# Kernel tuning notes

Measured on AMD Instinct MI355X. Metric: run time of the kernel, lower is better.

Reference implementation:

```python
import jax, jax.numpy as jnp
import numpy as np

N = 50000      # nodes per graph
E = 800000     # edges per graph
IN_DIM = 64
HIDDEN = 128
OUT_DIM = 2
P = 100000     # candidate residue pairs


def setup_inputs() -> dict:
    key = jax.random.key(0)
    ks = jax.random.split(key, 12)
    x1 = jax.random.normal(ks[0], (N, IN_DIM), dtype=jnp.float32)
    x2 = jax.random.normal(ks[1], (N, IN_DIM), dtype=jnp.float32)
    edge_index1 = jax.random.randint(ks[2], (2, E), 0, N, dtype=jnp.int64)
    edge_index2 = jax.random.randint(ks[3], (2, E), 0, N, dtype=jnp.int64)
    label = jax.random.randint(ks[4], (P, 2), 0, N, dtype=jnp.int64)
    s = 0.05
    W0 = jax.random.normal(ks[5], (IN_DIM, HIDDEN), dtype=jnp.float32) * s
    W1 = jax.random.normal(ks[6], (HIDDEN, HIDDEN), dtype=jnp.float32) * s
    W2 = jax.random.normal(ks[7], (HIDDEN, HIDDEN), dtype=jnp.float32) * s
    b0 = jnp.zeros((HIDDEN,), dtype=jnp.float32)
    b1 = jnp.zeros((HIDDEN,), dtype=jnp.float32)
    b2 = jnp.zeros((HIDDEN,), dtype=jnp.float32)
    fcW = jax.random.normal(ks[8], (2 * HIDDEN, OUT_DIM), dtype=jnp.float32) * s
    fcb = jnp.zeros((OUT_DIM,), dtype=jnp.float32)
    return {"x1": x1, "edge_index1": edge_index1, "x2": x2,
            "edge_index2": edge_index2, "label": label,
            "W0": W0, "b0": b0, "W1": W1, "b1": b1, "W2": W2, "b2": b2,
            "fcW": fcW, "fcb": fcb}


def gcn_conv(x, src, dst, W, b):
    """PyG GCNConv: linear, add self-loops, symmetric D^-1/2 (A+I) D^-1/2 aggregation."""
    n = x.shape[0]
    h = x @ W                                   # [n, out]
    loops = jnp.arange(n, dtype=src.dtype)
    src_sl = jnp.concatenate([src, loops])      # [E+n]
    dst_sl = jnp.concatenate([dst, loops])
    deg = jax.ops.segment_sum(jnp.ones_like(src_sl, dtype=h.dtype), dst_sl,
                              num_segments=n)
    dinv = jax.lax.rsqrt(jnp.maximum(deg, 1.0e-12))
    norm = dinv[src_sl] * dinv[dst_sl]          # [E+n]
    msgs = h[src_sl] * norm[:, None]            # gather + scale
    out = jax.ops.segment_sum(msgs, dst_sl, num_segments=n)  # scatter-add
    return out + b


def gcn_tower(x, edge_index, params):
    src, dst = edge_index[0], edge_index[1]
    for (W, b) in params:
        x = jax.nn.relu(gcn_conv(x, src, dst, W, b))
    return x


def reference(x1, edge_index1, x2, edge_index2, label,
              W0, b0, W1, b1, W2, b2, fcW, fcb):
    params = [(W0, b0), (W1, b1), (W2, b2)]
    x_ligand = gcn_tower(x1, edge_index1, params)    # shared GCN weights
    x_receptor = gcn_tower(x2, edge_index2, params)
    x = jnp.concatenate([x_ligand[label[:, 0]], x_receptor[label[:, 1]]], axis=1)
    return jax.nn.relu(x @ fcW + fcb)
```

## Files before the change

### kernel.cpp

```cpp
#include <hip/hip_runtime.h>
#include <math.h>



__global__ void histU_kernel(const int* __restrict__ d1, const int* __restrict__ d2,
                             int* __restrict__ cnt, int E, int N) {
    int i = blockIdx.x * blockDim.x + threadIdx.x;
    if (i < E) atomicAdd(&cnt[d1[i]], 1);
    else if (i < 2 * E) atomicAdd(&cnt[N + d2[i - E]], 1);
}

__global__ __launch_bounds__(256) void block_reduce_kernel(const int* __restrict__ cnt,
                                                           float* __restrict__ dinv,
                                                           int* __restrict__ blockSums, int NN) {
    int i = blockIdx.x * 256 + threadIdx.x;
    int v = 0;
    if (i < NN) {
        v = cnt[i];
        dinv[i] = 1.0f / sqrtf((float)(v + 1));
    }
    int s = v;
#pragma unroll
    for (int o = 32; o; o >>= 1) s += __shfl_down(s, o);
    __shared__ int ws[4];
    if ((threadIdx.x & 63) == 0) ws[threadIdx.x >> 6] = s;
    __syncthreads();
    if (threadIdx.x == 0) blockSums[blockIdx.x] = ws[0] + ws[1] + ws[2] + ws[3];
}

__global__ __launch_bounds__(1024) void scan_sums_kernel(const int* __restrict__ blockSums,
                                                         int* __restrict__ blockOff, int nb,
                                                         int* __restrict__ rowptr, int NN) {
    __shared__ int sh[1024];
    int t = threadIdx.x;
    int v = (t < nb) ? blockSums[t] : 0;
    sh[t] = v;
    __syncthreads();
    for (int o = 1; o < 1024; o <<= 1) {
        int u = (t >= o) ? sh[t - o] : 0;
        __syncthreads();
        sh[t] += u;
        __syncthreads();
    }
    if (t < nb) blockOff[t] = sh[t] - v;
    if (t == 1023) rowptr[NN] = sh[1023];
}

__global__ __launch_bounds__(256) void scan_write_kernel(const int* __restrict__ cnt,
                                                         const int* __restrict__ blockOff,
                                                         int* __restrict__ rowptr, int NN) {
    __shared__ int sh[256];
    int i = blockIdx.x * 256 + threadIdx.x;
    int t = threadIdx.x;
    int v = (i < NN) ? cnt[i] : 0;
    sh[t] = v;
    __syncthreads();
    for (int o = 1; o < 256; o <<= 1) {
        int u = (t >= o) ? sh[t - o] : 0;
        __syncthreads();
        sh[t] += u;
        __syncthreads();
    }
    if (i < NN) rowptr[i] = blockOff[blockIdx.x] + sh[t] - v;
}

__global__ void placeU_kernel(const int* __restrict__ s1, const int* __restrict__ d1,
                              const int* __restrict__ s2, const int* __restrict__ d2,
                              const int* __restrict__ rowptr, int* __restrict__ cnt,
                              int* __restrict__ csr, int E, int N) {
    int i = blockIdx.x * blockDim.x + threadIdx.x;
    int s, d;
    if (i < E)          { s = s1[i];         d = d1[i]; }
    else if (i < 2 * E) { s = s2[i - E] + N; d = d2[i - E] + N; }
    else return;
    int p = atomicSub(&cnt[d], 1);
    csr[rowptr[d] + p - 1] = s;
}


__global__ void agg64U_kernel(const float* __restrict__ x1, const float* __restrict__ x2,
                              const int* __restrict__ rowptr, const int* __restrict__ csr,
                              const float* __restrict__ dinv, float* __restrict__ S,
                              int NN, int N) {
    int w = blockIdx.x * (blockDim.x >> 6) + (threadIdx.x >> 6);
    int lane = threadIdx.x & 63;
    if (w >= NN) return;
    int beg = rowptr[w], end = rowptr[w + 1];
    const float* selfrow = (w < N) ? (x1 + (size_t)w * 64) : (x2 + (size_t)(w - N) * 64);
    float acc = dinv[w] * selfrow[lane];
    int e = beg;
    for (; e + 8 <= end; e += 8) {
        int s0 = csr[e], s1 = csr[e + 1], s2 = csr[e + 2], s3 = csr[e + 3];
        int s4 = csr[e + 4], s5 = csr[e + 5], s6 = csr[e + 6], s7 = csr[e + 7];
        const float* r0 = (s0 < N) ? (x1 + (size_t)s0 * 64) : (x2 + (size_t)(s0 - N) * 64);
        const float* r1 = (s1 < N) ? (x1 + (size_t)s1 * 64) : (x2 + (size_t)(s1 - N) * 64);
        const float* r2 = (s2 < N) ? (x1 + (size_t)s2 * 64) : (x2 + (size_t)(s2 - N) * 64);
        const float* r3 = (s3 < N) ? (x1 + (size_t)s3 * 64) : (x2 + (size_t)(s3 - N) * 64);
        const float* r4 = (s4 < N) ? (x1 + (size_t)s4 * 64) : (x2 + (size_t)(s4 - N) * 64);
        const float* r5 = (s5 < N) ? (x1 + (size_t)s5 * 64) : (x2 + (size_t)(s5 - N) * 64);
        const float* r6 = (s6 < N) ? (x1 + (size_t)s6 * 64) : (x2 + (size_t)(s6 - N) * 64);
        const float* r7 = (s7 < N) ? (x1 + (size_t)s7 * 64) : (x2 + (size_t)(s7 - N) * 64);
        float v0 = dinv[s0] * r0[lane];
        float v1 = dinv[s1] * r1[lane];
        float v2 = dinv[s2] * r2[lane];
        float v3 = dinv[s3] * r3[lane];
        float v4 = dinv[s4] * r4[lane];
        float v5 = dinv[s5] * r5[lane];
        float v6 = dinv[s6] * r6[lane];
        float v7 = dinv[s7] * r7[lane];
        acc += ((v0 + v1) + (v2 + v3)) + ((v4 + v5) + (v6 + v7));
    }
    for (; e < end; ++e) {
        int s = csr[e];
        const float* r = (s < N) ? (x1 + (size_t)s * 64) : (x2 + (size_t)(s - N) * 64);
        acc += dinv[s] * r[lane];
    }
    S[(size_t)w * 64 + lane] = acc;
}


__global__ void agg128_kernel(const float* __restrict__ Xf, const int* __restrict__ rowptr,
                              const int* __restrict__ csr, float* __restrict__ Sf, int NN) {
    int w = blockIdx.x * (blockDim.x >> 6) + (threadIdx.x >> 6);
    int lane = threadIdx.x & 63;
    if (w >= NN) return;
    const float2* X = (const float2*)Xf;
    float2* S = (float2*)Sf;
    int beg = rowptr[w], end = rowptr[w + 1];
    float2 self = X[(size_t)w * 64 + lane];
    float ax = self.x, ay = self.y;
    int e = beg;
    for (; e + 8 <= end; e += 8) {
        int s0 = csr[e], s1 = csr[e + 1], s2 = csr[e + 2], s3 = csr[e + 3];
        int s4 = csr[e + 4], s5 = csr[e + 5], s6 = csr[e + 6], s7 = csr[e + 7];
        float2 v0 = X[(size_t)s0 * 64 + lane];
        float2 v1 = X[(size_t)s1 * 64 + lane];
        float2 v2 = X[(size_t)s2 * 64 + lane];
        float2 v3 = X[(size_t)s3 * 64 + lane];
        float2 v4 = X[(size_t)s4 * 64 + lane];
        float2 v5 = X[(size_t)s5 * 64 + lane];
        float2 v6 = X[(size_t)s6 * 64 + lane];
        float2 v7 = X[(size_t)s7 * 64 + lane];
        ax += ((v0.x + v1.x) + (v2.x + v3.x)) + ((v4.x + v5.x) + (v6.x + v7.x));
        ay += ((v0.y + v1.y) + (v2.y + v3.y)) + ((v4.y + v5.y) + (v6.y + v7.y));
    }
    for (; e < end; ++e) {
        float2 v = X[(size_t)csr[e] * 64 + lane];
        ax += v.x; ay += v.y;
    }
    float2 r; r.x = ax; r.y = ay;
    S[(size_t)w * 64 + lane] = r;
}


template <int K>
__global__ __launch_bounds__(256) void gemm_relu(const float* __restrict__ A,
                                                 const float* __restrict__ W,
                                                 const float* __restrict__ B,
                                                 const float* __restrict__ dinv, int post,
                                                 float* __restrict__ C, int M) {
    const int BK = 32;
    __shared__ float As[BK][68];
    __shared__ float Ws[BK][128];

    int t = threadIdx.x;
    int tx = t & 31, ty = t >> 5;
    int row0 = blockIdx.x * 64;

    float acc[8][4];
#pragma unroll
    for (int i = 0; i < 8; ++i)
#pragma unroll
        for (int j = 0; j < 4; ++j) acc[i][j] = 0.f;

    for (int k0 = 0; k0 < K; k0 += BK) {
#pragma unroll
        for (int l = 0; l < 2; ++l) {
            int j = t + l * 256;
            int r = j >> 3, kq = j & 7;
            int gr = row0 + r; if (gr >= M) gr = M - 1;
            float4 v = *reinterpret_cast<const float4*>(A + (size_t)gr * K + k0 + kq * 4);
            As[kq * 4 + 0][r] = v.x;
            As[kq * 4 + 1][r] = v.y;
            As[kq * 4 + 2][r] = v.z;
            As[kq * 4 + 3][r] = v.w;
        }
#pragma unroll
        for (int l = 0; l < 4; ++l) {
            int j = t + l * 256;
            int k = j >> 5, c4 = j & 31;
            *reinterpret_cast<float4*>(&Ws[k][c4 * 4]) =
                *reinterpret_cast<const float4*>(W + (size_t)(k0 + k) * 128 + c4 * 4);
        }
        __syncthreads();
#pragma unroll
        for (int k = 0; k < BK; ++k) {
            float4 w0 = *reinterpret_cast<const float4*>(&Ws[k][tx * 4]);
            float4 a0 = *reinterpret_cast<const float4*>(&As[k][ty * 8]);
            float4 a1 = *reinterpret_cast<const float4*>(&As[k][ty * 8 + 4]);
            float a[8] = {a0.x, a0.y, a0.z, a0.w, a1.x, a1.y, a1.z, a1.w};
            float wv[4] = {w0.x, w0.y, w0.z, w0.w};
#pragma unroll
            for (int i = 0; i < 8; ++i)
#pragma unroll
                for (int j = 0; j < 4; ++j) acc[i][j] += a[i] * wv[j];
        }
        __syncthreads();
    }

    float4 bc = *reinterpret_cast<const float4*>(B + tx * 4);
#pragma unroll
    for (int i = 0; i < 8; ++i) {
        int r = row0 + ty * 8 + i;
        if (r < M) {
            float d = dinv[r];
            float po = post ? d : 1.0f;
            float4 v;
            v.x = fmaxf(acc[i][0] * d + bc.x, 0.f) * po;
            v.y = fmaxf(acc[i][1] * d + bc.y, 0.f) * po;
            v.z = fmaxf(acc[i][2] * d + bc.z, 0.f) * po;
            v.w = fmaxf(acc[i][3] * d + bc.w, 0.f) * po;
            *reinterpret_cast<float4*>(&C[(size_t)r * 128 + tx * 4]) = v;
        }
    }
}


__global__ void fc_kernel(const float* __restrict__ H3, const int* __restrict__ label,
                          const float* __restrict__ fcW, const float* __restrict__ fcb,
                          float* __restrict__ out, int P, int N) {
    int w = blockIdx.x * (blockDim.x >> 6) + (threadIdx.x >> 6);
    int lane = threadIdx.x & 63;
    if (w >= P) return;
    int l0 = label[2 * w], l1 = label[2 * w + 1] + N;
    float xl0 = H3[(size_t)l0 * 128 + lane];
    float xl1 = H3[(size_t)l0 * 128 + 64 + lane];
    float xr0 = H3[(size_t)l1 * 128 + lane];
    float xr1 = H3[(size_t)l1 * 128 + 64 + lane];
    float a0 = xl0 * fcW[lane * 2]             + xl1 * fcW[(64 + lane) * 2]
             + xr0 * fcW[(128 + lane) * 2]     + xr1 * fcW[(192 + lane) * 2];
    float a1 = xl0 * fcW[lane * 2 + 1]         + xl1 * fcW[(64 + lane) * 2 + 1]
             + xr0 * fcW[(128 + lane) * 2 + 1] + xr1 * fcW[(192 + lane) * 2 + 1];
#pragma unroll
    for (int o = 32; o; o >>= 1) {
        a0 += __shfl_xor(a0, o);
        a1 += __shfl_xor(a1, o);
    }
    if (lane == 0) {
        out[2 * w]     = fmaxf(a0 + fcb[0], 0.f);
        out[2 * w + 1] = fmaxf(a1 + fcb[1], 0.f);
    }
}


extern "C" void kernel_launch(void* const* d_in, const int* in_sizes, int n_in,
                              void* d_out, int out_size, void* d_ws, size_t ws_size,
                              hipStream_t stream) {
    const float* x1   = (const float*)d_in[0];
    const int*   e1   = (const int*)d_in[1];
    const float* x2   = (const float*)d_in[2];
    const int*   e2   = (const int*)d_in[3];
    const int*   label= (const int*)d_in[4];
    const float* W0   = (const float*)d_in[5];
    const float* b0   = (const float*)d_in[6];
    const float* W1   = (const float*)d_in[7];
    const float* b1   = (const float*)d_in[8];
    const float* W2   = (const float*)d_in[9];
    const float* b2   = (const float*)d_in[10];
    const float* fcW  = (const float*)d_in[11];
    const float* fcb  = (const float*)d_in[12];
    float* out = (float*)d_out;

    const int N = in_sizes[0] / 64;
    const int E = in_sizes[1] / 2;
    const int P = in_sizes[4] / 2;
    const int NN = 2 * N;
    const int NB = (NN + 255) / 256;

    char* ws = (char*)d_ws;
    size_t off = 0;
    auto alloc = [&](size_t bytes) -> void* {
        void* p = ws + off;
        off += (bytes + 255) & ~(size_t)255;
        return p;
    };
    int*   cnt      = (int*)alloc((size_t)NN * 4);
    int*   rowptr   = (int*)alloc((size_t)(NN + 1) * 4);
    float* dinv     = (float*)alloc((size_t)NN * 4);
    int*   csr      = (int*)alloc((size_t)2 * E * 4);
    int*   blockSums= (int*)alloc((size_t)NB * 4);
    int*   blockOff = (int*)alloc((size_t)NB * 4);
    float* S        = (float*)alloc((size_t)NN * 128 * 4);
    float* Xs       = (float*)alloc((size_t)NN * 128 * 4);

    hipMemsetAsync(cnt, 0, (size_t)NN * 4, stream);
    histU_kernel<<<(2 * E + 255) / 256, 256, 0, stream>>>(e1 + E, e2 + E, cnt, E, N);
    block_reduce_kernel<<<NB, 256, 0, stream>>>(cnt, dinv, blockSums, NN);
    scan_sums_kernel<<<1, 1024, 0, stream>>>(blockSums, blockOff, NB, rowptr, NN);
    scan_write_kernel<<<NB, 256, 0, stream>>>(cnt, blockOff, rowptr, NN);
    placeU_kernel<<<(2 * E + 255) / 256, 256, 0, stream>>>(e1, e1 + E, e2, e2 + E,
                                                           rowptr, cnt, csr, E, N);
    agg64U_kernel<<<(NN + 3) / 4, 256, 0, stream>>>(x1, x2, rowptr, csr, dinv, S, NN, N);
    gemm_relu<64><<<(NN + 63) / 64, 256, 0, stream>>>(S, W0, b0, dinv, 1, Xs, NN);
    agg128_kernel<<<(NN + 3) / 4, 256, 0, stream>>>(Xs, rowptr, csr, S, NN);
    gemm_relu<128><<<(NN + 63) / 64, 256, 0, stream>>>(S, W1, b1, dinv, 1, Xs, NN);
    agg128_kernel<<<(NN + 3) / 4, 256, 0, stream>>>(Xs, rowptr, csr, S, NN);
    gemm_relu<128><<<(NN + 63) / 64, 256, 0, stream>>>(S, W2, b2, dinv, 0, Xs, NN);

    fc_kernel<<<(P + 3) / 4, 256, 0, stream>>>(Xs, label, fcW, fcb, out, P, N);
}
```

Measured before the change: 611.2 us.

## Run GCN dense layers on bf16x3 MFMA with split hi/lo operands

Replaces the FP32 SIMT tiled GEMM with an MFMA 16x16x32 bf16 kernel. It keeps near-fp32 accuracy by splitting activations and weights into bf16 hi/lo pairs and summing three products. The aggregation kernels now write the hi/lo bf16 pair directly, and a small prep kernel splits and transposes the weights. The aggregation tails also become a predicated unrolled loop. This trades extra MFMA work and conversion arithmetic for tensor-core throughput, at some precision risk from the dropped lo*lo term.

```diff
diff --git a/kernel.cpp b/kernel.cpp
--- a/kernel.cpp
+++ b/kernel.cpp
@@ -1,6 +1,17 @@
 #include <hip/hip_runtime.h>
 #include <math.h>
 
+typedef __attribute__((ext_vector_type(8))) short bf16x8;
+typedef __attribute__((ext_vector_type(4))) float f32x4;
+
+__device__ inline unsigned short f2bf(float f) {
+    unsigned int u = __float_as_uint(f);
+    unsigned int r = u + 0x7fffu + ((u >> 16) & 1u);
+    return (unsigned short)(r >> 16);
+}
+__device__ inline float bf2f(unsigned short b) {
+    return __uint_as_float(((unsigned int)b) << 16);
+}
 
 
 __global__ void histU_kernel(const int* __restrict__ d1, const int* __restrict__ d2,
@@ -78,9 +89,30 @@
 }
 
 
+__global__ void prep_weights(const float* __restrict__ W0, const float* __restrict__ W1,
+                             const float* __restrict__ W2,
+                             unsigned short* __restrict__ W0h, unsigned short* __restrict__ W0l,
+                             unsigned short* __restrict__ W1h, unsigned short* __restrict__ W1l,
+                             unsigned short* __restrict__ W2h, unsigned short* __restrict__ W2l) {
+    const float* W; unsigned short *Wh, *Wl; int K;
+    if (blockIdx.x == 0)      { W = W0; Wh = W0h; Wl = W0l; K = 64; }
+    else if (blockIdx.x == 1) { W = W1; Wh = W1h; Wl = W1l; K = 128; }
+    else                      { W = W2; Wh = W2h; Wl = W2l; K = 128; }
+    for (int i = threadIdx.x; i < K * 128; i += 256) {
+        int k = i >> 7, c = i & 127;
+        float v = W[i];
+        unsigned short h = f2bf(v);
+        unsigned short l = f2bf(v - bf2f(h));
+        Wh[c * K + k] = h;
+        Wl[c * K + k] = l;
+    }
+}
+
+
 __global__ void agg64U_kernel(const float* __restrict__ x1, const float* __restrict__ x2,
                               const int* __restrict__ rowptr, const int* __restrict__ csr,
-                              const float* __restrict__ dinv, float* __restrict__ S,
+                              const float* __restrict__ dinv,
+                              unsigned short* __restrict__ Shi, unsigned short* __restrict__ Slo,
                               int NN, int N) {
     int w = blockIdx.x * (blockDim.x >> 6) + (threadIdx.x >> 6);
     int lane = threadIdx.x & 63;
@@ -89,7 +121,8 @@
     const float* selfrow = (w < N) ? (x1 + (size_t)w * 64) : (x2 + (size_t)(w - N) * 64);
     float acc = dinv[w] * selfrow[lane];
     int e = beg;
-    for (; e + 8 <= end; e += 8) {
+    int full_end = beg + ((end - beg) & ~7);
+    for (; e < full_end; e += 8) {
         int s0 = csr[e], s1 = csr[e + 1], s2 = csr[e + 2], s3 = csr[e + 3];
         int s4 = csr[e + 4], s5 = csr[e + 5], s6 = csr[e + 6], s7 = csr[e + 7];
         const float* r0 = (s0 < N) ? (x1 + (size_t)s0 * 64) : (x2 + (size_t)(s0 - N) * 64);
@@ -110,27 +143,37 @@
         float v7 = dinv[s7] * r7[lane];
         acc += ((v0 + v1) + (v2 + v3)) + ((v4 + v5) + (v6 + v7));
     }
-    for (; e < end; ++e) {
-        int s = csr[e];
-        const float* r = (s < N) ? (x1 + (size_t)s * 64) : (x2 + (size_t)(s - N) * 64);
-        acc += dinv[s] * r[lane];
-    }
-    S[(size_t)w * 64 + lane] = acc;
+    if (e < end) {
+#pragma unroll
+        for (int j = 0; j < 7; ++j) {
+            int a = e + j;
+            bool vld = a < end;
+            int s = csr[vld ? a : beg];
+            float wt = vld ? dinv[s] : 0.f;
+            const float* r = (s < N) ? (x1 + (size_t)s * 64) : (x2 + (size_t)(s - N) * 64);
+            acc += wt * r[lane];
+        }
+    }
+    unsigned short h = f2bf(acc);
+    Shi[(size_t)w * 64 + lane] = h;
+    Slo[(size_t)w * 64 + lane] = f2bf(acc - bf2f(h));
 }
 
 
 __global__ void agg128_kernel(const float* __restrict__ Xf, const int* __restrict__ rowptr,
-                              const int* __restrict__ csr, float* __restrict__ Sf, int NN) {
+                              const int* __restrict__ csr,
+                              unsigned short* __restrict__ Shi, unsigned short* __restrict__ Slo,
+                              int NN) {
     int w = blockIdx.x * (blockDim.x >> 6) + (threadIdx.x >> 6);
     int lane = threadIdx.x & 63;
     if (w >= NN) return;
     const float2* X = (const float2*)Xf;
-    float2* S = (float2*)Sf;
     int beg = rowptr[w], end = rowptr[w + 1];
     float2 self = X[(size_t)w * 64 + lane];
     float ax = self.x, ay = self.y;
     int e = beg;
-    for (; e + 8 <= end; e += 8) {
+    int full_end = beg + ((end - beg) & ~7);
+    for (; e < full_end; e += 8) {
         int s0 = csr[e], s1 = csr[e + 1], s2 = csr[e + 2], s3 = csr[e + 3];
         int s4 = csr[e + 4], s5 = csr[e + 5], s6 = csr[e + 6], s7 = csr[e + 7];
         float2 v0 = X[(size_t)s0 * 64 + lane];
@@ -144,83 +187,86 @@
         ax += ((v0.x + v1.x) + (v2.x + v3.x)) + ((v4.x + v5.x) + (v6.x + v7.x));
         ay += ((v0.y + v1.y) + (v2.y + v3.y)) + ((v4.y + v5.y) + (v6.y + v7.y));
     }
-    for (; e < end; ++e) {
-        float2 v = X[(size_t)csr[e] * 64 + lane];
-        ax += v.x; ay += v.y;
-    }
-    float2 r; r.x = ax; r.y = ay;
-    S[(size_t)w * 64 + lane] = r;
+    if (e < end) {
+#pragma unroll
+        for (int j = 0; j < 7; ++j) {
+            int a = e + j;
+            bool vld = a < end;
+            int s = csr[vld ? a : beg];
+            float m = vld ? 1.f : 0.f;
+            float2 v = X[(size_t)s * 64 + lane];
+            ax += m * v.x; ay += m * v.y;
+        }
+    }
+    unsigned short hx = f2bf(ax), hy = f2bf(ay);
+    ushort2 H; H.x = hx; H.y = hy;
+    ushort2 L; L.x = f2bf(ax - bf2f(hx)); L.y = f2bf(ay - bf2f(hy));
+    *reinterpret_cast<ushort2*>(Shi + (size_t)w * 128 + 2 * lane) = H;
+    *reinterpret_cast<ushort2*>(Slo + (size_t)w * 128 + 2 * lane) = L;
 }
 
 
 template <int K>
-__global__ __launch_bounds__(256) void gemm_relu(const float* __restrict__ A,
-                                                 const float* __restrict__ W,
-                                                 const float* __restrict__ B,
+__global__ __launch_bounds__(512) void gemm_mfma(const unsigned short* __restrict__ Ah,
+                                                 const unsigned short* __restrict__ Al,
+                                                 const unsigned short* __restrict__ WhT,
+                                                 const unsigned short* __restrict__ WlT,
+                                                 const float* __restrict__ bias,
                                                  const float* __restrict__ dinv, int post,
                                                  float* __restrict__ C, int M) {
-    const int BK = 32;
-    __shared__ float As[BK][68];
-    __shared__ float Ws[BK][128];
+    const int LDA = K + 8;
+    __shared__ unsigned short lds[2 * 128 * LDA];
+    unsigned short* ldsH = lds;
+    unsigned short* ldsL = lds + 128 * LDA;
 
     int t = threadIdx.x;
-    int tx = t & 31, ty = t >> 5;
-    int row0 = blockIdx.x * 64;
-
-    float acc[8][4];
-#pragma unroll
-    for (int i = 0; i < 8; ++i)
-#pragma unroll
-        for (int j = 0; j < 4; ++j) acc[i][j] = 0.f;
-
-    for (int k0 = 0; k0 < K; k0 += BK) {
-#pragma unroll
-        for (int l = 0; l < 2; ++l) {
-            int j = t + l * 256;
-            int r = j >> 3, kq = j & 7;
-            int gr = row0 + r; if (gr >= M) gr = M - 1;
-            float4 v = *reinterpret_cast<const float4*>(A + (size_t)gr * K + k0 + kq * 4);
-            As[kq * 4 + 0][r] = v.x;
-            As[kq * 4 + 1][r] = v.y;
-            As[kq * 4 + 2][r] = v.z;
-            As[kq * 4 + 3][r] = v.w;
-        }
-#pragma unroll
-        for (int l = 0; l < 4; ++l) {
-            int j = t + l * 256;
-            int k = j >> 5, c4 = j & 31;
-            *reinterpret_cast<float4*>(&Ws[k][c4 * 4]) =
-                *reinterpret_cast<const float4*>(W + (size_t)(k0 + k) * 128 + c4 * 4);
-        }
-        __syncthreads();
-#pragma unroll
-        for (int k = 0; k < BK; ++k) {
-            float4 w0 = *reinterpret_cast<const float4*>(&Ws[k][tx * 4]);
-            float4 a0 = *reinterpret_cast<const float4*>(&As[k][ty * 8]);
-            float4 a1 = *reinterpret_cast<const float4*>(&As[k][ty * 8 + 4]);
-            float a[8] = {a0.x, a0.y, a0.z, a0.w, a1.x, a1.y, a1.z, a1.w};
-            float wv[4] = {w0.x, w0.y, w0.z, w0.w};
-#pragma unroll
-            for (int i = 0; i < 8; ++i)
-#pragma unroll
-                for (int j = 0; j < 4; ++j) acc[i][j] += a[i] * wv[j];
-        }
-        __syncthreads();
-    }
-
-    float4 bc = *reinterpret_cast<const float4*>(B + tx * 4);
-#pragma unroll
-    for (int i = 0; i < 8; ++i) {
-        int r = row0 + ty * 8 + i;
-        if (r < M) {
-            float d = dinv[r];
-            float po = post ? d : 1.0f;
-            float4 v;
-            v.x = fmaxf(acc[i][0] * d + bc.x, 0.f) * po;
-            v.y = fmaxf(acc[i][1] * d + bc.y, 0.f) * po;
-            v.z = fmaxf(acc[i][2] * d + bc.z, 0.f) * po;
-            v.w = fmaxf(acc[i][3] * d + bc.w, 0.f) * po;
-            *reinterpret_cast<float4*>(&C[(size_t)r * 128 + tx * 4]) = v;
+    int lane = t & 63, wid = t >> 6;
+    int c16 = lane & 15, kq = (lane >> 4) * 8;
+    int row0 = blockIdx.x * 128;
+
+    bf16x8 wh[K / 32], wl[K / 32];
+    {
+        int col = wid * 16 + c16;
+#pragma unroll
+        for (int ks = 0; ks < K / 32; ++ks) {
+            wh[ks] = *reinterpret_cast<const bf16x8*>(WhT + (size_t)col * K + ks * 32 + kq);
+            wl[ks] = *reinterpret_cast<const bf16x8*>(WlT + (size_t)col * K + ks * 32 + kq);
+        }
+    }
+
+    const int CH = 128 * K / 8;
+    for (int c = t; c < CH; c += 512) {
+        int row = c / (K / 8), kb = c % (K / 8);
+        int gr = row0 + row; if (gr >= M) gr = M - 1;
+        *reinterpret_cast<bf16x8*>(ldsH + row * LDA + kb * 8) =
+            *reinterpret_cast<const bf16x8*>(Ah + (size_t)gr * K + kb * 8);
+        *reinterpret_cast<bf16x8*>(ldsL + row * LDA + kb * 8) =
+            *reinterpret_cast<const bf16x8*>(Al + (size_t)gr * K + kb * 8);
+    }
+    __syncthreads();
+
+    float bb = bias[wid * 16 + c16];
+#pragma unroll
+    for (int rt = 0; rt < 8; ++rt) {
+        f32x4 acc = {0.f, 0.f, 0.f, 0.f};
+        int abase = (rt * 16 + c16) * LDA + kq;
+#pragma unroll
+        for (int ks = 0; ks < K / 32; ++ks) {
+            bf16x8 ah = *reinterpret_cast<const bf16x8*>(ldsH + abase + ks * 32);
+            bf16x8 al = *reinterpret_cast<const bf16x8*>(ldsL + abase + ks * 32);
+            acc = __builtin_amdgcn_mfma_f32_16x16x32_bf16(ah, wh[ks], acc, 0, 0, 0);
+            acc = __builtin_amdgcn_mfma_f32_16x16x32_bf16(ah, wl[ks], acc, 0, 0, 0);
+            acc = __builtin_amdgcn_mfma_f32_16x16x32_bf16(al, wh[ks], acc, 0, 0, 0);
+        }
+#pragma unroll
+        for (int r = 0; r < 4; ++r) {
+            int gr = row0 + rt * 16 + (lane >> 4) * 4 + r;
+            if (gr < M) {
+                float d = dinv[gr];
+                float po = post ? d : 1.0f;
+                float v = fmaxf(acc[r] * d + bb, 0.f) * po;
+                C[(size_t)gr * 128 + wid * 16 + c16] = v;
+            }
         }
     }
 }
@@ -290,8 +336,19 @@
     int*   csr      = (int*)alloc((size_t)2 * E * 4);
     int*   blockSums= (int*)alloc((size_t)NB * 4);
     int*   blockOff = (int*)alloc((size_t)NB * 4);
-    float* S        = (float*)alloc((size_t)NN * 128 * 4);
+    unsigned short* Shi = (unsigned short*)alloc((size_t)NN * 128 * 2);
+    unsigned short* Slo = (unsigned short*)alloc((size_t)NN * 128 * 2);
     float* Xs       = (float*)alloc((size_t)NN * 128 * 4);
+    unsigned short* W0h = (unsigned short*)alloc(64 * 128 * 2);
+    unsigned short* W0l = (unsigned short*)alloc(64 * 128 * 2);
+    unsigned short* W1h = (unsigned short*)alloc(128 * 128 * 2);
+    unsigned short* W1l = (unsigned short*)alloc(128 * 128 * 2);
+    unsigned short* W2h = (unsigned short*)alloc(128 * 128 * 2);
+    unsigned short* W2l = (unsigned short*)alloc(128 * 128 * 2);
+
+    const int GB = (NN + 127) / 128;
+
+    prep_weights<<<3, 256, 0, stream>>>(W0, W1, W2, W0h, W0l, W1h, W1l, W2h, W2l);
 
     hipMemsetAsync(cnt, 0, (size_t)NN * 4, stream);
     histU_kernel<<<(2 * E + 255) / 256, 256, 0, stream>>>(e1 + E, e2 + E, cnt, E, N);
@@ -300,12 +357,12 @@
     scan_write_kernel<<<NB, 256, 0, stream>>>(cnt, blockOff, rowptr, NN);
     placeU_kernel<<<(2 * E + 255) / 256, 256, 0, stream>>>(e1, e1 + E, e2, e2 + E,
                                                            rowptr, cnt, csr, E, N);
-    agg64U_kernel<<<(NN + 3) / 4, 256, 0, stream>>>(x1, x2, rowptr, csr, dinv, S, NN, N);
-    gemm_relu<64><<<(NN + 63) / 64, 256, 0, stream>>>(S, W0, b0, dinv, 1, Xs, NN);
-    agg128_kernel<<<(NN + 3) / 4, 256, 0, stream>>>(Xs, rowptr, csr, S, NN);
-    gemm_relu<128><<<(NN + 63) / 64, 256, 0, stream>>>(S, W1, b1, dinv, 1, Xs, NN);
-    agg128_kernel<<<(NN + 3) / 4, 256, 0, stream>>>(Xs, rowptr, csr, S, NN);
-    gemm_relu<128><<<(NN + 63) / 64, 256, 0, stream>>>(S, W2, b2, dinv, 0, Xs, NN);
+    agg64U_kernel<<<(NN + 3) / 4, 256, 0, stream>>>(x1, x2, rowptr, csr, dinv, Shi, Slo, NN, N);
+    gemm_mfma<64><<<GB, 512, 0, stream>>>(Shi, Slo, W0h, W0l, b0, dinv, 1, Xs, NN);
+    agg128_kernel<<<(NN + 3) / 4, 256, 0, stream>>>(Xs, rowptr, csr, Shi, Slo, NN);
+    gemm_mfma<128><<<GB, 512, 0, stream>>>(Shi, Slo, W1h, W1l, b1, dinv, 1, Xs, NN);
+    agg128_kernel<<<(NN + 3) / 4, 256, 0, stream>>>(Xs, rowptr, csr, Shi, Slo, NN);
+    gemm_mfma<128><<<GB, 512, 0, stream>>>(Shi, Slo, W2h, W2l, b2, dinv, 0, Xs, NN);
 
     fc_kernel<<<(P + 3) / 4, 256, 0, stream>>>(Xs, label, fcW, fcb, out, P, N);
 }
```

After: 584.6 us. -4.4%, faster.
